# Kernel tuning notes

Hardware: AMD Instinct MI355X
Metric: run time of the kernel (lower is better)

## Reference

```python
import jax, jax.numpy as jnp
import numpy as np

NU, EU = 40000, 640000          # user-graph nodes / edges
B, T, NW, ET = 64, 16, 30, 60    # users, tweets/user, words/tweet, edges/tweet
NT = B * T * NW                  # 30720 tweet word-nodes
NTE = B * T * ET                 # 61440 tweet edges
NSEG_T = B * T                   # 1024 tweet segments


def gcn_conv(x, src, dst, W, b, N):
    """PyG GCNConv: x@W, add self loops, sym deg-normalize, scatter-add, +b."""
    x = x @ W
    loop = jnp.arange(N)
    s = jnp.concatenate([src, loop])
    d = jnp.concatenate([dst, loop])
    deg = jax.ops.segment_sum(jnp.ones_like(d, dtype=x.dtype), d, num_segments=N)
    dinv = jnp.where(deg > 0, jax.lax.rsqrt(deg), 0.0)
    norm = dinv[s] * dinv[d]                     # [E+N]
    out = jax.ops.segment_sum(x[s] * norm[:, None], d, num_segments=N)
    return out + b


def att_pool(x, seg, nseg, W1, b1, W2, b2):
    """AttentionalAggregation: gate_nn = Linear->Linear, segment softmax, weighted sum."""
    gate = (x @ W1 + b1) @ W2 + b2               # [N, C]
    m = jax.ops.segment_max(gate, seg, num_segments=nseg)
    e = jnp.exp(gate - m[seg])
    s = jax.ops.segment_sum(e, seg, num_segments=nseg)
    a = e / (s[seg] + 1e-16)
    return jax.ops.segment_sum(a * x, seg, num_segments=nseg)  # [nseg, C]


def gru_last(x_seq, W_ih, W_hh, b_ih, b_hh):
    """torch.nn.GRU, 1 layer; x_seq [B,T,C] -> final hidden [B,C]."""
    C = W_hh.shape[1]
    h0 = jnp.zeros((x_seq.shape[0], C), x_seq.dtype)
    def step(h, x):
        gi = x @ W_ih.T + b_ih
        gh = h @ W_hh.T + b_hh
        ir, iz, inn = jnp.split(gi, 3, axis=-1)
        hr, hz, hn = jnp.split(gh, 3, axis=-1)
        r = jax.nn.sigmoid(ir + hr)
        z = jax.nn.sigmoid(iz + hz)
        n = jnp.tanh(inn + r * hn)
        return (1.0 - z) * n + z * h, None
    hT, _ = jax.lax.scan(step, h0, jnp.swapaxes(x_seq, 0, 1))
    return hT


def setup_inputs():
    ks = jax.random.split(jax.random.key(0), 24)
    def rn(i, shape, s=1.0):
        return jax.random.normal(ks[i], shape, dtype=jnp.float32) * s
    z = lambda n_: jnp.zeros((n_,), jnp.float32)
    inp = {}
    inp["user_x"] = rn(0, (NU, 128))
    inp["user_feats"] = rn(1, (B, 32))
    inp["tweet_x"] = rn(2, (NT, 768))
    inp["Wu0"] = rn(3, (128, 128), 0.1); inp["bu0"] = z(128)
    inp["Wu1"] = rn(4, (128, 128), 0.1); inp["bu1"] = z(128)
    inp["Wgu1"] = rn(5, (128, 128), 0.1); inp["bgu1"] = z(128)
    inp["Wgu2"] = rn(6, (128, 128), 0.1); inp["bgu2"] = z(128)
    inp["Wt0"] = rn(7, (768, 256), 0.05); inp["bt0"] = z(256)
    inp["Wt1"] = rn(8, (256, 128), 0.1); inp["bt1"] = z(128)
    inp["Wgt1"] = rn(9, (128, 128), 0.1); inp["bgt1"] = z(128)
    inp["Wgt2"] = rn(10, (128, 128), 0.1); inp["bgt2"] = z(128)
    inp["W_ih"] = rn(11, (384, 128), 0.1); inp["b_ih"] = z(384)
    inp["W_hh"] = rn(12, (384, 128), 0.1); inp["b_hh"] = z(384)
    inp["Wd0"] = rn(13, (288, 256), 0.1); inp["bd0"] = z(256)
    inp["Wd1"] = rn(14, (256, 64), 0.1); inp["bd1"] = z(64)
    inp["Wp"] = rn(15, (64, 1), 0.1); inp["bp"] = z(1)
    inp["user_edge_index"] = jax.random.randint(ks[16], (2, EU), 0, NU)
    local = jax.random.randint(ks[17], (2, NTE), 0, NW)
    offs = jnp.repeat(jnp.arange(NSEG_T) * NW, ET)   # edges stay inside each tweet
    inp["tweet_edge_index"] = local + offs[None, :]
    inp["user_batch"] = jnp.arange(NU) // (NU // B)  # contiguous per-user segments (ptr)
    inp["tweet_batch"] = jnp.arange(NT) // NW        # contiguous per-tweet segments (ptr)
    return inp


def reference(user_x, user_feats, tweet_x,
              Wu0, bu0, Wu1, bu1, Wgu1, bgu1, Wgu2, bgu2,
              Wt0, bt0, Wt1, bt1, Wgt1, bgt1, Wgt2, bgt2,
              W_ih, b_ih, W_hh, b_hh,
              Wd0, bd0, Wd1, bd1, Wp, bp,
              user_edge_index, tweet_edge_index, user_batch, tweet_batch):
    h = jax.nn.relu(gcn_conv(user_x, user_edge_index[0], user_edge_index[1], Wu0, bu0, NU))
    h = jax.nn.relu(gcn_conv(h, user_edge_index[0], user_edge_index[1], Wu1, bu1, NU))
    user_pool = att_pool(h, user_batch, B, Wgu1, bgu1, Wgu2, bgu2)        # [B,128]
    g = jax.nn.relu(gcn_conv(tweet_x, tweet_edge_index[0], tweet_edge_index[1], Wt0, bt0, NT))
    g = jax.nn.relu(gcn_conv(g, tweet_edge_index[0], tweet_edge_index[1], Wt1, bt1, NT))
    tweet_pool = att_pool(g, tweet_batch, NSEG_T, Wgt1, bgt1, Wgt2, bgt2)  # [B*T,128]
    tweet_seq = tweet_pool.reshape(B, T, 128)
    tweet_h = gru_last(tweet_seq, W_ih, W_hh, b_ih, b_hh)                 # [B,128]
    # head
    full = jnp.concatenate([user_feats, user_pool, tweet_h], axis=1)      # [B,288]
    full = jax.nn.relu(full @ Wd0 + bd0)
    full = jax.nn.relu(full @ Wd1 + bd1)
    return jax.nn.sigmoid(full @ Wp + bp)                                 # [B,1]
```

## Files before the change

kernel.cpp:

```cpp
#include <hip/hip_runtime.h>
#include <hip/hip_bf16.h>

#define NU 40000
#define EU 640000
#define BB 64
#define TT 16
#define NW 30
#define NTNODES 30720
#define NTE 61440
#define NSEG_T 1024
#define NCHUNK 16
#define NBU 157
#define NBT 120

typedef __attribute__((ext_vector_type(8))) short bf16x8;
typedef __attribute__((ext_vector_type(4))) float f32x4;

__device__ __forceinline__ unsigned short f2bf(float x) {
    union { float f; unsigned u; } v; v.f = x;
    unsigned r = v.u + 0x7FFFu + ((v.u >> 16) & 1u);
    return (unsigned short)(r >> 16);
}
__device__ __forceinline__ float bf2f(unsigned short u) {
    union { unsigned u; float f; } v; v.u = (unsigned)u << 16; return v.f;
}
__device__ __forceinline__ void gld16(const unsigned short* g, unsigned short* l) {
    __builtin_amdgcn_global_load_lds(
        (const __attribute__((address_space(1))) void*)g,
        (__attribute__((address_space(3))) void*)l, 16, 0, 0);
}

__global__ void k_zeroint(int* __restrict__ p, int n) {
    int i = blockIdx.x * blockDim.x + threadIdx.x;
    if (i < n) p[i] = 0;
}

__global__ void k_hist2(const int* __restrict__ ue_dst, const int* __restrict__ te_dst,
                        int* __restrict__ hist_u, int* __restrict__ hist_t) {
    int i = blockIdx.x * blockDim.x + threadIdx.x;
    if (i < EU) atomicAdd(&hist_u[ue_dst[i]], 1);
    else if (i < EU + NTE) atomicAdd(&hist_t[te_dst[i - EU]], 1);
}

__global__ __launch_bounds__(256) void k_scan_a2(const int* __restrict__ hist_u,
                                                 int* __restrict__ bsum_u,
                                                 int* __restrict__ bsum_t) {
    __shared__ int red[256];
    int b = blockIdx.x, t = threadIdx.x;
    const int* h; int* bs; int n, lb;
    if (b < NBU) { h = hist_u;      bs = bsum_u; n = NU;      lb = b; }
    else         { h = hist_u + NU; bs = bsum_t; n = NTNODES; lb = b - NBU; }
    int i = lb * 256 + t;
    red[t] = (i < n) ? h[i] : 0;
    __syncthreads();
    for (int off = 128; off; off >>= 1) {
        if (t < off) red[t] += red[t + off];
        __syncthreads();
    }
    if (t == 0) bs[lb] = red[0];
}

__global__ __launch_bounds__(256) void k_scan_b2(int* __restrict__ bsum_u,
                                                 int* __restrict__ bsum_t) {
    __shared__ int s[256];
    int t = threadIdx.x;
    int* bs = blockIdx.x ? bsum_t : bsum_u;
    int nb  = blockIdx.x ? NBT : NBU;
    s[t] = (t < nb) ? bs[t] : 0;
    __syncthreads();
    for (int off = 1; off < 256; off <<= 1) {
        int v = (t >= off) ? s[t - off] : 0;
        __syncthreads();
        s[t] += v;
        __syncthreads();
    }
    if (t < nb) bs[t] = (t == 0) ? 0 : s[t - 1];
}

__global__ __launch_bounds__(256) void k_scan_c2(const int* __restrict__ hist_u,
                                                 const int* __restrict__ bsum_u,
                                                 const int* __restrict__ bsum_t,
                                                 int* __restrict__ ptr_u, int* __restrict__ fill_u,
                                                 int* __restrict__ ptr_t, int* __restrict__ fill_t,
                                                 float* __restrict__ dinv_u) {
    __shared__ int s[256];
    int b = blockIdx.x, t = threadIdx.x;
    const int *h, *bs; int *ptr, *fill; int n, lb; float* dv;
    if (b < NBU) { h = hist_u;      bs = bsum_u; ptr = ptr_u; fill = fill_u; n = NU;      lb = b;       dv = dinv_u; }
    else         { h = hist_u + NU; bs = bsum_t; ptr = ptr_t; fill = fill_t; n = NTNODES; lb = b - NBU; dv = dinv_u + NU; }
    int i = lb * 256 + t;
    int hv = (i < n) ? h[i] : 0;
    s[t] = hv;
    __syncthreads();
    for (int off = 1; off < 256; off <<= 1) {
        int v = (t >= off) ? s[t - off] : 0;
        __syncthreads();
        s[t] += v;
        __syncthreads();
    }
    if (i < n) {
        int excl = bs[lb] + s[t] - hv;
        ptr[i] = excl;
        fill[i] = excl;
        dv[i] = rsqrtf((float)hv + 1.0f);
        if (i == n - 1) ptr[n] = excl + hv;
    }
}

__global__ void k_place2(const int* __restrict__ ue_src, const int* __restrict__ ue_dst,
                         const int* __restrict__ te_src, const int* __restrict__ te_dst,
                         int* __restrict__ fill_u, int* __restrict__ esrc_u,
                         int* __restrict__ fill_t, int* __restrict__ esrc_t) {
    int e = blockIdx.x * blockDim.x + threadIdx.x;
    if (e < EU) {
        int pos = atomicAdd(&fill_u[ue_dst[e]], 1);
        esrc_u[pos] = ue_src[e];
    } else if (e < EU + NTE) {
        int e2 = e - EU;
        int pos = atomicAdd(&fill_t[te_dst[e2]], 1);
        esrc_t[pos] = te_src[e2];
    }
}

__device__ __forceinline__ void pack_one(const float* __restrict__ W,
                                         unsigned short* __restrict__ out,
                                         int f, int K, int N, int trans) {
    int j = f & 7;
    int chunk = f >> 3;
    int c = chunk & 511;
    int panel = chunk >> 9;
    int KS = K >> 5;
    int ks = panel % KS;
    int bn = panel / KS;
    int n = bn * 128 + (c & 127);
    int k = ks * 32 + (c >> 7) * 8 + j;
    float v = trans ? W[(size_t)n * K + k] : W[(size_t)k * N + n];
    out[f] = f2bf(v);
}

__global__ void k_packall(const float* __restrict__ Wu0, const float* __restrict__ Wu1,
                          const float* __restrict__ Wgu1, const float* __restrict__ Wgu2,
                          const float* __restrict__ Wt0, const float* __restrict__ Wt1,
                          const float* __restrict__ Wgt1, const float* __restrict__ Wgt2,
                          const float* __restrict__ Wih,
                          const float* __restrict__ Whh, float* __restrict__ whhT,
                          unsigned short* __restrict__ pk) {
    int f = blockIdx.x * blockDim.x + threadIdx.x;
    if (f < 16384)        pack_one(Wu0,  pk + 0,      f,          128, 128, 0);
    else if (f < 32768)   pack_one(Wu1,  pk + 16384,  f - 16384,  128, 128, 0);
    else if (f < 49152)   pack_one(Wgu1, pk + 32768,  f - 32768,  128, 128, 0);
    else if (f < 65536)   pack_one(Wgu2, pk + 49152,  f - 49152,  128, 128, 0);
    else if (f < 262144)  pack_one(Wt0,  pk + 65536,  f - 65536,  768, 256, 0);
    else if (f < 294912)  pack_one(Wt1,  pk + 262144, f - 262144, 256, 128, 0);
    else if (f < 311296)  pack_one(Wgt1, pk + 294912, f - 294912, 128, 128, 0);
    else if (f < 327680)  pack_one(Wgt2, pk + 311296, f - 311296, 128, 128, 0);
    else if (f < 376832)  pack_one(Wih,  pk + 327680, f - 327680, 128, 384, 1);
    else if (f < 425984) {
        int j2 = f - 376832;
        int r = j2 >> 7, k2 = j2 & 127;
        whhT[k2 * 384 + r] = Whh[j2];
    }
}

template<bool AF32>
__device__ __forceinline__ void mgemm_body(const void* __restrict__ Araw,
                                           const unsigned short* __restrict__ Bpk,
                                           const float* __restrict__ bias,
                                           const float* __restrict__ dscale,
                                           void* __restrict__ Craw,
                                           int M, int K, int N, int flags,
                                           int bm, int bn,
                                           unsigned short* Alds, unsigned short* Blds) {
    constexpr int AST = AF32 ? 260 : 256;
    int tid = threadIdx.x, lane = tid & 63, w = tid >> 6;
    int wr = (w >> 1) * 16, wc = (w & 1) * 64;
    int l15 = lane & 15, lk = lane >> 4;

    f32x4 acc[4];
#pragma unroll
    for (int n = 0; n < 4; ++n) acc[n] = (f32x4){0.f, 0.f, 0.f, 0.f};

    const unsigned short* Bpanel = Bpk + (size_t)bn * (K >> 5) * 4096;
    int KS64 = K >> 6;

    for (int ks = 0; ks < KS64; ++ks) {
        int k0 = ks * 64;
        {
            const unsigned short* bg = Bpanel + (size_t)ks * 8192;
#pragma unroll
            for (int q = 0; q < 4; ++q) {
                int off = (w * 4 + q) * 512;
                gld16(bg + off + lane * 8, &Blds[off]);
            }
        }
        if (AF32) {
            const float* A = (const float*)Araw;
#pragma unroll
            for (int p = 0; p < 2; ++p) {
                int f4 = p * 256 + tid;
                int row = f4 >> 4;
                int kq  = f4 & 15;
                float4 av = *(const float4*)(A + (size_t)(bm * 32 + row) * K + k0 + kq * 4);
                unsigned lo = (unsigned)f2bf(av.x) | ((unsigned)f2bf(av.y) << 16);
                unsigned hi = (unsigned)f2bf(av.z) | ((unsigned)f2bf(av.w) << 16);
                int off = (kq >> 1) * AST + row * 8 + (kq & 1) * 4;
                *(uint2*)&Alds[off] = make_uint2(lo, hi);
            }
        } else {
            const unsigned short* A = (const unsigned short*)Araw;
            int kblk = 2 * w + (lane >> 5);
            int row = lane & 31;
            gld16(A + (size_t)(bm * 32 + row) * K + k0 + kblk * 8,
                  &Alds[w * 512]);
        }
        __syncthreads();
#pragma unroll
        for (int h = 0; h < 2; ++h) {
            int kb = h * 4 + lk;
            bf16x8 a = *(const bf16x8*)&Alds[kb * AST + (wr + l15) * 8];
            bf16x8 b[4];
#pragma unroll
            for (int n = 0; n < 4; ++n)
                b[n] = *(const bf16x8*)&Blds[kb * 1024 + (wc + n * 16 + l15) * 8];
#pragma unroll
            for (int n = 0; n < 4; ++n)
                acc[n] = __builtin_amdgcn_mfma_f32_16x16x32_bf16(a, b[n], acc[n], 0, 0, 0);
        }
        __syncthreads();
    }

    int grow0 = bm * 32 + wr + lk * 4;
#pragma unroll
    for (int i = 0; i < 4; ++i) {
        int grow = grow0 + i;
        float ds = dscale ? dscale[grow] : 1.f;
#pragma unroll
        for (int n = 0; n < 4; ++n) {
            int gcol = bn * 128 + wc + n * 16 + l15;
            float v = acc[n][i] * ds;
            if (flags & 1) v += bias[gcol];
            if (flags & 2) v = fmaxf(v, 0.f);
            if (flags & 4) ((float*)Craw)[(size_t)grow * N + gcol] = v;
            else ((unsigned short*)Craw)[(size_t)grow * N + gcol] = f2bf(v);
        }
    }
}

template<bool AF32>
__global__ __launch_bounds__(256) void k_mgemm(const void* __restrict__ Araw,
                                               const unsigned short* __restrict__ Bpk,
                                               const float* __restrict__ bias,
                                               const float* __restrict__ dscale,
                                               void* __restrict__ Craw,
                                               int M, int K, int N, int flags) {
    constexpr int AST = AF32 ? 260 : 256;
    __shared__ unsigned short Alds[8 * AST];
    __shared__ unsigned short Blds[8192];
    if (blockIdx.x * 32 >= M) return;
    mgemm_body<AF32>(Araw, Bpk, bias, dscale, Craw, M, K, N, flags,
                     blockIdx.x, blockIdx.y, Alds, Blds);
}

template<bool AF32>
__global__ __launch_bounds__(256) void k_mgemm_dual(
        const void* __restrict__ A0, const unsigned short* __restrict__ B0,
        const float* __restrict__ ds0, void* __restrict__ C0, int M0, int K0, int N0,
        const void* __restrict__ A1, const unsigned short* __restrict__ B1,
        const float* __restrict__ ds1, void* __restrict__ C1, int M1, int K1, int N1,
        int bnSplit) {
    constexpr int AST = AF32 ? 260 : 256;
    __shared__ unsigned short Alds[8 * AST];
    __shared__ unsigned short Blds[8192];
    int bn = blockIdx.y, bm = blockIdx.x;
    if (bn < bnSplit) {
        if (bm * 32 >= M0) return;
        mgemm_body<AF32>(A0, B0, (const float*)nullptr, ds0, C0, M0, K0, N0, 0,
                         bm, bn, Alds, Blds);
    } else {
        if (bm * 32 >= M1) return;
        mgemm_body<AF32>(A1, B1, (const float*)nullptr, ds1, C1, M1, K1, N1, 0,
                         bm, bn - bnSplit, Alds, Blds);
    }
}

__device__ __forceinline__ void gatepair_body(const unsigned short* __restrict__ X,
                                              const unsigned short* __restrict__ W1,
                                              const float* __restrict__ b1,
                                              const unsigned short* __restrict__ W2,
                                              const float* __restrict__ b2,
                                              unsigned short* __restrict__ outp,
                                              int bm,
                                              unsigned short* Ax, unsigned short* Wl) {
    int tid = threadIdx.x, lane = tid & 63, w = tid >> 6;
    int wr = (w >> 1) * 32, wc = (w & 1) * 64;
    int l15 = lane & 15, lk = lane >> 4;

#pragma unroll
    for (int q = 0; q < 4; ++q) {
        int pl = w * 4 + q;
        gld16(X + (size_t)(bm * 64 + lane) * 128 + pl * 8, &Ax[pl * 512]);
    }

    f32x4 acc[2][4];
#pragma unroll
    for (int m = 0; m < 2; ++m)
#pragma unroll
        for (int n = 0; n < 4; ++n) acc[m][n] = (f32x4){0.f, 0.f, 0.f, 0.f};

    for (int ks = 0; ks < 2; ++ks) {
        const unsigned short* wp = W1 + ks * 8192;
#pragma unroll
        for (int q = 0; q < 4; ++q) {
            int off = (w * 4 + q) * 512;
            gld16(wp + off + lane * 8, &Wl[off]);
        }
        __syncthreads();
#pragma unroll
        for (int h = 0; h < 2; ++h) {
            int kb = h * 4 + lk;
            bf16x8 a[2], b[4];
#pragma unroll
            for (int m = 0; m < 2; ++m)
                a[m] = *(const bf16x8*)&Ax[(ks * 8 + kb) * 512 + (wr + m * 16 + l15) * 8];
#pragma unroll
            for (int n = 0; n < 4; ++n)
                b[n] = *(const bf16x8*)&Wl[kb * 1024 + (wc + n * 16 + l15) * 8];
#pragma unroll
            for (int m = 0; m < 2; ++m)
#pragma unroll
                for (int n = 0; n < 4; ++n)
                    acc[m][n] = __builtin_amdgcn_mfma_f32_16x16x32_bf16(a[m], b[n], acc[m][n], 0, 0, 0);
        }
        __syncthreads();
    }

#pragma unroll
    for (int m = 0; m < 2; ++m)
#pragma unroll
        for (int n = 0; n < 4; ++n) {
            int col = wc + n * 16 + l15;
            float bv = b1[col];
#pragma unroll
            for (int i = 0; i < 4; ++i) {
                int row = wr + m * 16 + lk * 4 + i;
                float v = acc[m][n][i] + bv;
                Ax[(col >> 3) * 512 + row * 8 + (col & 7)] = f2bf(v);
            }
        }
    __syncthreads();

#pragma unroll
    for (int m = 0; m < 2; ++m)
#pragma unroll
        for (int n = 0; n < 4; ++n) acc[m][n] = (f32x4){0.f, 0.f, 0.f, 0.f};
    for (int ks = 0; ks < 2; ++ks) {
        const unsigned short* wp = W2 + ks * 8192;
#pragma unroll
        for (int q = 0; q < 4; ++q) {
            int off = (w * 4 + q) * 512;
            gld16(wp + off + lane * 8, &Wl[off]);
        }
        __syncthreads();
#pragma unroll
        for (int h = 0; h < 2; ++h) {
            int kb = h * 4 + lk;
            bf16x8 a[2], b[4];
#pragma unroll
            for (int m = 0; m < 2; ++m)
                a[m] = *(const bf16x8*)&Ax[(ks * 8 + kb) * 512 + (wr + m * 16 + l15) * 8];
#pragma unroll
            for (int n = 0; n < 4; ++n)
                b[n] = *(const bf16x8*)&Wl[kb * 1024 + (wc + n * 16 + l15) * 8];
#pragma unroll
            for (int m = 0; m < 2; ++m)
#pragma unroll
                for (int n = 0; n < 4; ++n)
                    acc[m][n] = __builtin_amdgcn_mfma_f32_16x16x32_bf16(a[m], b[n], acc[m][n], 0, 0, 0);
        }
        __syncthreads();
    }

#pragma unroll
    for (int m = 0; m < 2; ++m)
#pragma unroll
        for (int n = 0; n < 4; ++n) {
            int col = wc + n * 16 + l15;
            float bv = b2[col];
#pragma unroll
            for (int i = 0; i < 4; ++i) {
                int row = bm * 64 + wr + m * 16 + lk * 4 + i;
                float v = acc[m][n][i] + bv;
                outp[(size_t)row * 128 + col] = f2bf(v);
            }
        }
}

__global__ __launch_bounds__(256) void k_gatepair2(
        const unsigned short* __restrict__ X0, const unsigned short* __restrict__ W10,
        const float* __restrict__ b10, const unsigned short* __restrict__ W20,
        const float* __restrict__ b20, unsigned short* __restrict__ O0, int nb0,
        const unsigned short* __restrict__ X1, const unsigned short* __restrict__ W11,
        const float* __restrict__ b11, const unsigned short* __restrict__ W21,
        const float* __restrict__ b21, unsigned short* __restrict__ O1) {
    __shared__ unsigned short Ax[16 * 512];
    __shared__ unsigned short Wl[8192];
    int b = blockIdx.x;
    if (b < nb0) gatepair_body(X0, W10, b10, W20, b20, O0, b, Ax, Wl);
    else         gatepair_body(X1, W11, b11, W21, b21, O1, b - nb0, Ax, Wl);
}

__device__ __forceinline__ void gagg_body(const unsigned short* __restrict__ y,
                                          const int* __restrict__ ptr,
                                          const int* __restrict__ esrc,
                                          const float* __restrict__ dinv,
                                          const float* __restrict__ bias,
                                          unsigned short* __restrict__ ob,
                                          int idx, int nch, int lane) {
    int v = idx / nch, ch = idx - v * nch;
    int C = nch << 7;
    int c0 = (ch << 7) + lane * 2;
    unsigned yv = *(const unsigned*)(y + (size_t)v * C + c0);
    float a0 = bf2f((unsigned short)yv);
    float a1 = bf2f((unsigned short)(yv >> 16));
    int e = ptr[v], e1 = ptr[v + 1];
    for (; e + 3 < e1; e += 4) {
        int s0 = esrc[e], s1 = esrc[e + 1], s2 = esrc[e + 2], s3 = esrc[e + 3];
        unsigned w0 = *(const unsigned*)(y + (size_t)s0 * C + c0);
        unsigned w1 = *(const unsigned*)(y + (size_t)s1 * C + c0);
        unsigned w2 = *(const unsigned*)(y + (size_t)s2 * C + c0);
        unsigned w3 = *(const unsigned*)(y + (size_t)s3 * C + c0);
        a0 += bf2f((unsigned short)w0) + bf2f((unsigned short)w1)
            + bf2f((unsigned short)w2) + bf2f((unsigned short)w3);
        a1 += bf2f((unsigned short)(w0 >> 16)) + bf2f((unsigned short)(w1 >> 16))
            + bf2f((unsigned short)(w2 >> 16)) + bf2f((unsigned short)(w3 >> 16));
    }
    for (; e < e1; ++e) {
        int s0 = esrc[e];
        unsigned w0 = *(const unsigned*)(y + (size_t)s0 * C + c0);
        a0 += bf2f((unsigned short)w0);
        a1 += bf2f((unsigned short)(w0 >> 16));
    }
    float dv = dinv[v];
    a0 = fmaxf(dv * a0 + bias[c0], 0.f);
    a1 = fmaxf(dv * a1 + bias[c0 + 1], 0.f);
    *(unsigned*)(ob + (size_t)v * C + c0) = (unsigned)f2bf(a0) | ((unsigned)f2bf(a1) << 16);
}

__global__ __launch_bounds__(256) void k_gagg2(
        const unsigned short* __restrict__ y0, const int* __restrict__ ptr0,
        const int* __restrict__ esrc0, const float* __restrict__ dinv0,
        const float* __restrict__ bias0, unsigned short* __restrict__ ob0, int N0, int nch0,
        const unsigned short* __restrict__ y1, const int* __restrict__ ptr1,
        const int* __restrict__ esrc1, const float* __restrict__ dinv1,
        const float* __restrict__ bias1, unsigned short* __restrict__ ob1, int N1, int nch1) {
    int idx = blockIdx.x * 4 + (threadIdx.x >> 6);
    int lane = threadIdx.x & 63;
    int T0 = N0 * nch0;
    if (idx < T0) gagg_body(y0, ptr0, esrc0, dinv0, bias0, ob0, idx, nch0, lane);
    else {
        idx -= T0;
        if (idx < N1 * nch1) gagg_body(y1, ptr1, esrc1, dinv1, bias1, ob1, idx, nch1, lane);
    }
}

__global__ __launch_bounds__(128) void k_attpool(const unsigned short* __restrict__ x,
                                                 const unsigned short* __restrict__ gate,
                                                 unsigned short* __restrict__ outb, int S) {
    int seg = blockIdx.x;
    int c = threadIdx.x;
    size_t base = (size_t)seg * S * 128 + c;
    float m = -1e30f;
    for (int n = 0; n < S; ++n) m = fmaxf(m, bf2f(gate[base + (size_t)n * 128]));
    float se = 0.f, acc = 0.f;
    for (int n = 0; n < S; ++n) {
        float g = bf2f(gate[base + (size_t)n * 128]);
        float e = expf(g - m);
        se += e;
        acc += e * bf2f(x[base + (size_t)n * 128]);
    }
    outb[(size_t)seg * 128 + c] = f2bf(acc / (se + 1e-16f));
}

__global__ __launch_bounds__(256) void k_pool_pmax(const unsigned short* __restrict__ gate,
                                                   float* __restrict__ pmax, int S) {
    int seg = blockIdx.x, ch = blockIdx.y;
    int c = threadIdx.x & 127, j = threadIdx.x >> 7;
    int csz = (S + NCHUNK - 1) / NCHUNK;
    int n0 = ch * csz, n1 = min(S, n0 + csz);
    size_t base = (size_t)seg * S * 128 + c;
    float m = -1e30f;
    for (int n = n0 + j; n < n1; n += 2)
        m = fmaxf(m, bf2f(gate[base + (size_t)n * 128]));
    __shared__ float red[2][128];
    red[j][c] = m;
    __syncthreads();
    if (j == 0)
        pmax[((size_t)seg * NCHUNK + ch) * 128 + c] = fmaxf(red[0][c], red[1][c]);
}

__global__ __launch_bounds__(256) void k_pool_psum(const unsigned short* __restrict__ x,
                                                   const unsigned short* __restrict__ gate,
                                                   const float* __restrict__ pmax,
                                                   float* __restrict__ pse,
                                                   float* __restrict__ pacc, int S) {
    int seg = blockIdx.x, ch = blockIdx.y;
    int c = threadIdx.x & 127, j = threadIdx.x >> 7;
    int csz = (S + NCHUNK - 1) / NCHUNK;
    int n0 = ch * csz, n1 = min(S, n0 + csz);
    size_t base = (size_t)seg * S * 128 + c;
    float m = -1e30f;
#pragma unroll
    for (int ch2 = 0; ch2 < NCHUNK; ++ch2)
        m = fmaxf(m, pmax[((size_t)seg * NCHUNK + ch2) * 128 + c]);
    float se = 0.f, acc = 0.f;
    for (int n = n0 + j; n < n1; n += 2) {
        float g = bf2f(gate[base + (size_t)n * 128]);
        float e = expf(g - m);
        se += e;
        acc += e * bf2f(x[base + (size_t)n * 128]);
    }
    __shared__ float rs[2][128], ra[2][128];
    rs[j][c] = se; ra[j][c] = acc;
    __syncthreads();
    if (j == 0) {
        size_t o = ((size_t)seg * NCHUNK + ch) * 128 + c;
        pse[o]  = rs[0][c] + rs[1][c];
        pacc[o] = ra[0][c] + ra[1][c];
    }
}

__global__ __launch_bounds__(128) void k_pool_final(const float* __restrict__ pse,
                                                    const float* __restrict__ pacc,
                                                    float* __restrict__ out) {
    int seg = blockIdx.x, c = threadIdx.x;
    float se = 0.f, acc = 0.f;
    for (int ch = 0; ch < NCHUNK; ++ch) {
        size_t o = ((size_t)seg * NCHUNK + ch) * 128 + c;
        se += pse[o];
        acc += pacc[o];
    }
    out[(size_t)seg * 128 + c] = acc / (se + 1e-16f);
}

__global__ __launch_bounds__(768) void k_gru_rec(const float* __restrict__ gi,
                                                 const float* __restrict__ whhT,
                                                 const float* __restrict__ bhh,
                                                 float* __restrict__ hT) {
    __shared__ float hs[128];
    __shared__ float ph[768];
    int b = blockIdx.x, t = threadIdx.x;
    int half = (t >= 384) ? 1 : 0;
    int j = t - half * 384;
    float w[64];
#pragma unroll
    for (int i = 0; i < 64; ++i)
        w[i] = whhT[(half * 64 + i) * 384 + j];
    float chr = 0.f, chz = 0.f, chn = 0.f;
    if (t < 128) {
        hs[t] = 0.f;
        chr = bhh[t]; chz = bhh[128 + t]; chn = bhh[256 + t];
    }
    __syncthreads();
    for (int step = 0; step < TT; ++step) {
        float a0 = 0.f, a1 = 0.f, a2 = 0.f, a3 = 0.f;
        const float* hbase = hs + half * 64;
#pragma unroll
        for (int i = 0; i < 64; i += 4) {
            float4 hv = *(const float4*)(hbase + i);
            a0 += hv.x * w[i + 0];
            a1 += hv.y * w[i + 1];
            a2 += hv.z * w[i + 2];
            a3 += hv.w * w[i + 3];
        }
        ph[t] = (a0 + a1) + (a2 + a3);
        __syncthreads();
        float hnew = 0.f;
        if (t < 128) {
            const float* girow = gi + ((size_t)b * TT + step) * 384;
            float hr = ph[t] + ph[t + 384] + chr;
            float hz = ph[128 + t] + ph[512 + t] + chz;
            float hn = ph[256 + t] + ph[640 + t] + chn;
            float ir = girow[t], iz = girow[128 + t], in = girow[256 + t];
            float r = 1.f / (1.f + expf(-(ir + hr)));
            float z = 1.f / (1.f + expf(-(iz + hz)));
            float n = tanhf(in + r * hn);
            hnew = (1.f - z) * n + z * hs[t];
        }
        __syncthreads();
        if (t < 128) hs[t] = hnew;
        __syncthreads();
    }
    if (t < 128) hT[(size_t)b * 128 + t] = hs[t];
}

__global__ __launch_bounds__(256) void k_head(const float* __restrict__ uf,
                                              const float* __restrict__ up,
                                              const float* __restrict__ th,
                                              const float* __restrict__ Wd0, const float* __restrict__ bd0,
                                              const float* __restrict__ Wd1, const float* __restrict__ bd1,
                                              const float* __restrict__ Wp, const float* __restrict__ bp,
                                              float* __restrict__ out) {
    __shared__ float in0[288], l1[256], l2[64];
    int b = blockIdx.x, t = threadIdx.x;
    if (t < 32) in0[t] = uf[b * 32 + t];
    else if (t < 160) in0[t] = up[b * 128 + (t - 32)];
    if (t < 128) in0[160 + t] = th[b * 128 + t];
    __syncthreads();
    float acc = bd0[t];
    for (int k = 0; k < 288; ++k) acc += in0[k] * Wd0[k * 256 + t];
    l1[t] = fmaxf(acc, 0.f);
    __syncthreads();
    if (t < 64) {
        float a2 = bd1[t];
        for (int k = 0; k < 256; ++k) a2 += l1[k] * Wd1[k * 64 + t];
        l2[t] = fmaxf(a2, 0.f);
    }
    __syncthreads();
    if (t < 64) {
        float p = l2[t] * Wp[t];
        for (int off = 32; off; off >>= 1) p += __shfl_down(p, off, 64);
        if (t == 0) out[b] = 1.f / (1.f + expf(-(p + bp[0])));
    }
}

extern "C" void kernel_launch(void* const* d_in, const int* in_sizes, int n_in,
                              void* d_out, int out_size, void* d_ws, size_t ws_size,
                              hipStream_t stream) {
    const float* user_x     = (const float*)d_in[0];
    const float* user_feats = (const float*)d_in[1];
    const float* tweet_x    = (const float*)d_in[2];
    const float* Wu0 = (const float*)d_in[3];  const float* bu0 = (const float*)d_in[4];
    const float* Wu1 = (const float*)d_in[5];  const float* bu1 = (const float*)d_in[6];
    const float* Wgu1 = (const float*)d_in[7]; const float* bgu1 = (const float*)d_in[8];
    const float* Wgu2 = (const float*)d_in[9]; const float* bgu2 = (const float*)d_in[10];
    const float* Wt0 = (const float*)d_in[11]; const float* bt0 = (const float*)d_in[12];
    const float* Wt1 = (const float*)d_in[13]; const float* bt1 = (const float*)d_in[14];
    const float* Wgt1 = (const float*)d_in[15]; const float* bgt1 = (const float*)d_in[16];
    const float* Wgt2 = (const float*)d_in[17]; const float* bgt2 = (const float*)d_in[18];
    const float* W_ih = (const float*)d_in[19]; const float* b_ih = (const float*)d_in[20];
    const float* W_hh = (const float*)d_in[21]; const float* b_hh = (const float*)d_in[22];
    const float* Wd0 = (const float*)d_in[23]; const float* bd0 = (const float*)d_in[24];
    const float* Wd1 = (const float*)d_in[25]; const float* bd1 = (const float*)d_in[26];
    const float* Wp  = (const float*)d_in[27]; const float* bp  = (const float*)d_in[28];
    const int* ue = (const int*)d_in[29];
    const int* te = (const int*)d_in[30];
    const int* ue_src = ue, *ue_dst = ue + EU;
    const int* te_src = te, *te_dst = te + NTE;

    float* ws = (float*)d_ws;
    size_t o = 0;
    float* dinv_u = ws + o;     o += NU;
    float* dinv_t = ws + o;     o += NTNODES;
    float* user_pool = ws + o;  o += (size_t)BB * 128;
    float* tweet_h = ws + o;    o += (size_t)BB * 128;
    float* whhT = ws + o;       o += 128 * 384;
    float* gi = ws + o;         o += (size_t)NSEG_T * 384;
    float* pmax = ws + o;       o += 131072;
    float* pse = ws + o;        o += 131072;
    float* pacc = ws + o;       o += 131072;
    int* iw = (int*)(ws + o);
    int* hist_u = iw;
    int* hist_t = iw + NU;
    int* ptr_u  = iw + NU + NTNODES;
    int* fill_u = ptr_u + NU + 1;
    int* esrc_u = fill_u + NU;
    int* ptr_t  = esrc_u + EU;
    int* fill_t = ptr_t + NTNODES + 1;
    int* esrc_t = fill_t + NTNODES;
    int* bsum_u = esrc_t + NTE;
    int* bsum_t = bsum_u + 256;
    unsigned short* pk = (unsigned short*)(((uintptr_t)(bsum_t + 256) + 15) & ~(uintptr_t)15);
    unsigned short* pWu0  = pk;
    unsigned short* pWu1  = pWu0  + 16384;
    unsigned short* pWgu1 = pWu1  + 16384;
    unsigned short* pWgu2 = pWgu1 + 16384;
    unsigned short* pWt0  = pWgu2 + 16384;
    unsigned short* pWt1  = pWt0  + 196608;
    unsigned short* pWgt1 = pWt1  + 32768;
    unsigned short* pWgt2 = pWgt1 + 16384;
    unsigned short* pWih  = pWgt2 + 16384;
    unsigned short* arena = (unsigned short*)(((uintptr_t)(pWih + 49152) + 15) & ~(uintptr_t)15);
    const size_t SLOT = (size_t)NTNODES * 256;
    unsigned short* P0 = arena;
    unsigned short* P1 = P0 + SLOT;
    unsigned short* P2 = P1 + SLOT;
    unsigned short* P3 = P2 + SLOT;
    unsigned short* tpool_bf = P3 + SLOT;
    float* out = (float*)d_out;

    dim3 b256(256);
    const float* ND = nullptr;

    hipLaunchKernelGGL(k_packall, dim3((425984 + 255) / 256), b256, 0, stream,
                       Wu0, Wu1, Wgu1, Wgu2, Wt0, Wt1, Wgt1, Wgt2, W_ih, W_hh, whhT, pk);

    hipLaunchKernelGGL(k_zeroint, dim3((NU + NTNODES + 255) / 256), b256, 0, stream,
                       hist_u, NU + NTNODES);
    hipLaunchKernelGGL(k_hist2, dim3((EU + NTE + 255) / 256), b256, 0, stream,
                       ue_dst, te_dst, hist_u, hist_t);
    hipLaunchKernelGGL(k_scan_a2, dim3(NBU + NBT), b256, 0, stream, hist_u, bsum_u, bsum_t);
    hipLaunchKernelGGL(k_scan_b2, dim3(2), b256, 0, stream, bsum_u, bsum_t);
    hipLaunchKernelGGL(k_scan_c2, dim3(NBU + NBT), b256, 0, stream,
                       hist_u, bsum_u, bsum_t, ptr_u, fill_u, ptr_t, fill_t, dinv_u);
    hipLaunchKernelGGL(k_place2, dim3((EU + NTE + 255) / 256), b256, 0, stream,
                       ue_src, ue_dst, te_src, te_dst, fill_u, esrc_u, fill_t, esrc_t);

    hipLaunchKernelGGL(HIP_KERNEL_NAME(k_mgemm_dual<true>), dim3(NU / 32, 3), b256, 0, stream,
                       (const void*)tweet_x, pWt0, dinv_t, (void*)P0, NTNODES, 768, 256,
                       (const void*)user_x,  pWu0, dinv_u, (void*)P2, NU,      128, 128,
                       2);
    hipLaunchKernelGGL(k_gagg2, dim3((NTNODES * 2 + NU + 3) / 4), b256, 0, stream,
                       P0, ptr_t, esrc_t, dinv_t, bt0, P1, NTNODES, 2,
                       P2, ptr_u, esrc_u, dinv_u, bu0, P3, NU, 1);
    hipLaunchKernelGGL(HIP_KERNEL_NAME(k_mgemm_dual<false>), dim3(NU / 32, 2), b256, 0, stream,
                       (const void*)P1, pWt1, dinv_t, (void*)P2, NTNODES, 256, 128,
                       (const void*)P3, pWu1, dinv_u, (void*)P0, NU,      128, 128,
                       1);
    hipLaunchKernelGGL(k_gagg2, dim3((NTNODES + NU + 3) / 4), b256, 0, stream,
                       P2, ptr_t, esrc_t, dinv_t, bt1, P1, NTNODES, 1,
                       P0, ptr_u, esrc_u, dinv_u, bu1, P3, NU, 1);
    hipLaunchKernelGGL(k_gatepair2, dim3(NU / 64 + NTNODES / 64), b256, 0, stream,
                       P3, pWgu1, bgu1, pWgu2, bgu2, P0, NU / 64,
                       P1, pWgt1, bgt1, pWgt2, bgt2, P2);

    hipLaunchKernelGGL(k_pool_pmax, dim3(BB, NCHUNK), b256, 0, stream, P0, pmax, NU / BB);
    hipLaunchKernelGGL(k_pool_psum, dim3(BB, NCHUNK), b256, 0, stream,
                       P3, P0, pmax, pse, pacc, NU / BB);
    hipLaunchKernelGGL(k_pool_final, dim3(BB), dim3(128), 0, stream, pse, pacc, user_pool);
    hipLaunchKernelGGL(k_attpool, dim3(NSEG_T), dim3(128), 0, stream,
                       P1, P2, tpool_bf, NW);

    hipLaunchKernelGGL(HIP_KERNEL_NAME(k_mgemm<false>), dim3(NSEG_T / 32, 3), b256, 0, stream,
                       (const void*)tpool_bf, pWih, b_ih, ND, (void*)gi, NSEG_T, 128, 384, 5);
    hipLaunchKernelGGL(k_gru_rec, dim3(BB), dim3(768), 0, stream,
                       gi, whhT, b_hh, tweet_h);

    hipLaunchKernelGGL(k_head, dim3(BB), b256, 0, stream,
                       user_feats, user_pool, tweet_h,
                       Wd0, bd0, Wd1, bd1, Wp, bp, out);
}
```

Measured before the change: 330.6 us.

## Double-buffer GEMM K-loop in LDS and split graph aggregation into 64-channel chunks

The MFMA GEMM body now walks K in 32-wide steps with two LDS buffers. It prefetches the next A and B tiles (and holds the fp32 A values in registers until after the MFMAs) while computing on the current ones, so there is one barrier per step instead of two. Separately, the GCN aggregation kernel gives each wavefront 64 channels with one bf16 per lane instead of 128 channels with two, doubling the number of waves. This is meant to hide global load latency and raise parallelism in the gather, at the cost of more loop iterations and narrower, less efficient gather loads.

```diff
diff --git a/kernel.cpp b/kernel.cpp
--- a/kernel.cpp
+++ b/kernel.cpp
@@ -172,6 +172,7 @@
                                            int bm, int bn,
                                            unsigned short* Alds, unsigned short* Blds) {
     constexpr int AST = AF32 ? 260 : 256;
+    constexpr int ABUF = 4 * AST;
     int tid = threadIdx.x, lane = tid & 63, w = tid >> 6;
     int wr = (w >> 1) * 16, wc = (w & 1) * 64;
     int l15 = lane & 15, lk = lane >> 4;
@@ -180,51 +181,67 @@
 #pragma unroll
     for (int n = 0; n < 4; ++n) acc[n] = (f32x4){0.f, 0.f, 0.f, 0.f};
 
-    const unsigned short* Bpanel = Bpk + (size_t)bn * (K >> 5) * 4096;
-    int KS64 = K >> 6;
-
-    for (int ks = 0; ks < KS64; ++ks) {
-        int k0 = ks * 64;
+    int KS = K >> 5;
+    const unsigned short* Bpanel = Bpk + (size_t)bn * KS * 4096;
+    const float* Af = (const float*)Araw;
+    const unsigned short* Ab = (const unsigned short*)Araw;
+    int arow32 = tid >> 3, akq = tid & 7;
+
+    {
+        const unsigned short* bg = Bpanel;
+#pragma unroll
+        for (int q = 0; q < 2; ++q) {
+            int i = w * 2 + q;
+            gld16(bg + i * 512 + lane * 8, &Blds[i * 512]);
+        }
+        if (AF32) {
+            float4 av = *(const float4*)(Af + (size_t)(bm * 32 + arow32) * K + akq * 4);
+            unsigned lo = (unsigned)f2bf(av.x) | ((unsigned)f2bf(av.y) << 16);
+            unsigned hi = (unsigned)f2bf(av.z) | ((unsigned)f2bf(av.w) << 16);
+            *(uint2*)&Alds[(akq >> 1) * AST + arow32 * 8 + (akq & 1) * 4] = make_uint2(lo, hi);
+        } else if (w < 2) {
+            gld16(Ab + (size_t)(bm * 32 + (lane & 31)) * K + (2 * w + (lane >> 5)) * 8,
+                  &Alds[w * 512]);
+        }
+    }
+    __syncthreads();
+
+    for (int ks = 0; ks < KS; ++ks) {
+        int cur = ks & 1, nxt = cur ^ 1;
+        bool have = (ks + 1 < KS);
+        float4 av;
+        if (have) {
+            const unsigned short* bg = Bpanel + (size_t)(ks + 1) * 4096;
+            unsigned short* Bn = Blds + nxt * 4096;
+#pragma unroll
+            for (int q = 0; q < 2; ++q) {
+                int i = w * 2 + q;
+                gld16(bg + i * 512 + lane * 8, &Bn[i * 512]);
+            }
+            if (AF32) {
+                av = *(const float4*)(Af + (size_t)(bm * 32 + arow32) * K + (ks + 1) * 32 + akq * 4);
+            } else if (w < 2) {
+                gld16(Ab + (size_t)(bm * 32 + (lane & 31)) * K + (ks + 1) * 32 + (2 * w + (lane >> 5)) * 8,
+                      &Alds[nxt * ABUF + w * 512]);
+            }
+        }
         {
-            const unsigned short* bg = Bpanel + (size_t)ks * 8192;
-#pragma unroll
-            for (int q = 0; q < 4; ++q) {
-                int off = (w * 4 + q) * 512;
-                gld16(bg + off + lane * 8, &Blds[off]);
-            }
-        }
-        if (AF32) {
-            const float* A = (const float*)Araw;
-#pragma unroll
-            for (int p = 0; p < 2; ++p) {
-                int f4 = p * 256 + tid;
-                int row = f4 >> 4;
-                int kq  = f4 & 15;
-                float4 av = *(const float4*)(A + (size_t)(bm * 32 + row) * K + k0 + kq * 4);
-                unsigned lo = (unsigned)f2bf(av.x) | ((unsigned)f2bf(av.y) << 16);
-                unsigned hi = (unsigned)f2bf(av.z) | ((unsigned)f2bf(av.w) << 16);
-                int off = (kq >> 1) * AST + row * 8 + (kq & 1) * 4;
-                *(uint2*)&Alds[off] = make_uint2(lo, hi);
-            }
-        } else {
-            const unsigned short* A = (const unsigned short*)Araw;
-            int kblk = 2 * w + (lane >> 5);
-            int row = lane & 31;
-            gld16(A + (size_t)(bm * 32 + row) * K + k0 + kblk * 8,
-                  &Alds[w * 512]);
-        }
-        __syncthreads();
-#pragma unroll
-        for (int h = 0; h < 2; ++h) {
-            int kb = h * 4 + lk;
-            bf16x8 a = *(const bf16x8*)&Alds[kb * AST + (wr + l15) * 8];
+            const unsigned short* Ac = Alds + cur * ABUF;
+            const unsigned short* Bc = Blds + cur * 4096;
+            bf16x8 a = *(const bf16x8*)&Ac[lk * AST + (wr + l15) * 8];
             bf16x8 b[4];
 #pragma unroll
             for (int n = 0; n < 4; ++n)
-                b[n] = *(const bf16x8*)&Blds[kb * 1024 + (wc + n * 16 + l15) * 8];
+                b[n] = *(const bf16x8*)&Bc[lk * 1024 + (wc + n * 16 + l15) * 8];
 #pragma unroll
             for (int n = 0; n < 4; ++n)
                 acc[n] = __builtin_amdgcn_mfma_f32_16x16x32_bf16(a, b[n], acc[n], 0, 0, 0);
+        }
+        if (AF32 && have) {
+            unsigned lo = (unsigned)f2bf(av.x) | ((unsigned)f2bf(av.y) << 16);
+            unsigned hi = (unsigned)f2bf(av.z) | ((unsigned)f2bf(av.w) << 16);
+            *(uint2*)&Alds[nxt * ABUF + (akq >> 1) * AST + arow32 * 8 + (akq & 1) * 4] =
+                make_uint2(lo, hi);
         }
         __syncthreads();
     }
@@ -254,8 +271,8 @@
                                                void* __restrict__ Craw,
                                                int M, int K, int N, int flags) {
     constexpr int AST = AF32 ? 260 : 256;
-    __shared__ unsigned short Alds[8 * AST];
-    __shared__ unsigned short Blds[8192];
+    __shared__ unsigned short Alds[2 * 4 * AST];
+    __shared__ unsigned short Blds[2 * 4096];
     if (blockIdx.x * 32 >= M) return;
     mgemm_body<AF32>(Araw, Bpk, bias, dscale, Craw, M, K, N, flags,
                      blockIdx.x, blockIdx.y, Alds, Blds);
@@ -269,8 +286,8 @@
         const float* __restrict__ ds1, void* __restrict__ C1, int M1, int K1, int N1,
         int bnSplit) {
     constexpr int AST = AF32 ? 260 : 256;
-    __shared__ unsigned short Alds[8 * AST];
-    __shared__ unsigned short Blds[8192];
+    __shared__ unsigned short Alds[2 * 4 * AST];
+    __shared__ unsigned short Blds[2 * 4096];
     int bn = blockIdx.y, bm = blockIdx.x;
     if (bn < bnSplit) {
         if (bm * 32 >= M0) return;
@@ -415,35 +432,24 @@
                                           const float* __restrict__ dinv,
                                           const float* __restrict__ bias,
                                           unsigned short* __restrict__ ob,
-                                          int idx, int nch, int lane) {
-    int v = idx / nch, ch = idx - v * nch;
-    int C = nch << 7;
-    int c0 = (ch << 7) + lane * 2;
-    unsigned yv = *(const unsigned*)(y + (size_t)v * C + c0);
-    float a0 = bf2f((unsigned short)yv);
-    float a1 = bf2f((unsigned short)(yv >> 16));
+                                          int idx, int nch64, int lane) {
+    int v = idx / nch64, ch = idx - v * nch64;
+    int C = nch64 << 6;
+    int c0 = (ch << 6) + lane;
+    float a0 = bf2f(y[(size_t)v * C + c0]);
     int e = ptr[v], e1 = ptr[v + 1];
     for (; e + 3 < e1; e += 4) {
         int s0 = esrc[e], s1 = esrc[e + 1], s2 = esrc[e + 2], s3 = esrc[e + 3];
-        unsigned w0 = *(const unsigned*)(y + (size_t)s0 * C + c0);
-        unsigned w1 = *(const unsigned*)(y + (size_t)s1 * C + c0);
-        unsigned w2 = *(const unsigned*)(y + (size_t)s2 * C + c0);
-        unsigned w3 = *(const unsigned*)(y + (size_t)s3 * C + c0);
-        a0 += bf2f((unsigned short)w0) + bf2f((unsigned short)w1)
-            + bf2f((unsigned short)w2) + bf2f((unsigned short)w3);
-        a1 += bf2f((unsigned short)(w0 >> 16)) + bf2f((unsigned short)(w1 >> 16))
-            + bf2f((unsigned short)(w2 >> 16)) + bf2f((unsigned short)(w3 >> 16));
-    }
-    for (; e < e1; ++e) {
-        int s0 = esrc[e];
-        unsigned w0 = *(const unsigned*)(y + (size_t)s0 * C + c0);
-        a0 += bf2f((unsigned short)w0);
-        a1 += bf2f((unsigned short)(w0 >> 16));
-    }
+        float x0 = bf2f(y[(size_t)s0 * C + c0]);
+        float x1 = bf2f(y[(size_t)s1 * C + c0]);
+        float x2 = bf2f(y[(size_t)s2 * C + c0]);
+        float x3 = bf2f(y[(size_t)s3 * C + c0]);
+        a0 += (x0 + x1) + (x2 + x3);
+    }
+    for (; e < e1; ++e)
+        a0 += bf2f(y[(size_t)esrc[e] * C + c0]);
     float dv = dinv[v];
-    a0 = fmaxf(dv * a0 + bias[c0], 0.f);
-    a1 = fmaxf(dv * a1 + bias[c0 + 1], 0.f);
-    *(unsigned*)(ob + (size_t)v * C + c0) = (unsigned)f2bf(a0) | ((unsigned)f2bf(a1) << 16);
+    ob[(size_t)v * C + c0] = f2bf(fmaxf(dv * a0 + bias[c0], 0.f));
 }
 
 __global__ __launch_bounds__(256) void k_gagg2(
@@ -709,16 +715,16 @@
                        (const void*)tweet_x, pWt0, dinv_t, (void*)P0, NTNODES, 768, 256,
                        (const void*)user_x,  pWu0, dinv_u, (void*)P2, NU,      128, 128,
                        2);
-    hipLaunchKernelGGL(k_gagg2, dim3((NTNODES * 2 + NU + 3) / 4), b256, 0, stream,
-                       P0, ptr_t, esrc_t, dinv_t, bt0, P1, NTNODES, 2,
-                       P2, ptr_u, esrc_u, dinv_u, bu0, P3, NU, 1);
+    hipLaunchKernelGGL(k_gagg2, dim3((NTNODES * 4 + NU * 2 + 3) / 4), b256, 0, stream,
+                       P0, ptr_t, esrc_t, dinv_t, bt0, P1, NTNODES, 4,
+                       P2, ptr_u, esrc_u, dinv_u, bu0, P3, NU, 2);
     hipLaunchKernelGGL(HIP_KERNEL_NAME(k_mgemm_dual<false>), dim3(NU / 32, 2), b256, 0, stream,
                        (const void*)P1, pWt1, dinv_t, (void*)P2, NTNODES, 256, 128,
                        (const void*)P3, pWu1, dinv_u, (void*)P0, NU,      128, 128,
                        1);
-    hipLaunchKernelGGL(k_gagg2, dim3((NTNODES + NU + 3) / 4), b256, 0, stream,
-                       P2, ptr_t, esrc_t, dinv_t, bt1, P1, NTNODES, 1,
-                       P0, ptr_u, esrc_u, dinv_u, bu1, P3, NU, 1);
+    hipLaunchKernelGGL(k_gagg2, dim3(((NTNODES + NU) * 2 + 3) / 4), b256, 0, stream,
+                       P2, ptr_t, esrc_t, dinv_t, bt1, P1, NTNODES, 2,
+                       P0, ptr_u, esrc_u, dinv_u, bu1, P3, NU, 2);
     hipLaunchKernelGGL(k_gatepair2, dim3(NU / 64 + NTNODES / 64), b256, 0, stream,
                        P3, pWgu1, bgu1, pWgu2, bgu2, P0, NU / 64,
                        P1, pWgt1, bgt1, pWgt2, bgt2, P2);
```

Result: slower. 414.0 us (+25.2%).
